# Kernel tuning notes

Measured on AMD Instinct MI355X. Metric: run time of the kernel, lower is better.

## Reference

```python
import jax, jax.numpy as jnp
import numpy as np
import math

B, S, D, H, PD = 2, 2048, 1024, 16, 3
DK = D // H          # 64
SP = S // H          # 128, required so physics_scores matches scores shape


def setup_inputs() -> dict:
    key = jax.random.key(0)
    ks = jax.random.split(key, 16)
    sc = 0.02
    return {
        "query": jax.random.normal(ks[0], (B, S, D), jnp.float32),
        "key_in": jax.random.normal(ks[1], (B, S, D), jnp.float32),
        "value": jax.random.normal(ks[2], (B, S, D), jnp.float32),
        "physics_info": jax.random.normal(ks[3], (B, SP, PD), jnp.float32),
        "Wq": jax.random.normal(ks[4], (D, D), jnp.float32) * sc,
        "bq": jnp.zeros((D,), jnp.float32),
        "Wk": jax.random.normal(ks[5], (D, D), jnp.float32) * sc,
        "bk": jnp.zeros((D,), jnp.float32),
        "Wv": jax.random.normal(ks[6], (D, D), jnp.float32) * sc,
        "bv": jnp.zeros((D,), jnp.float32),
        "Wo": jax.random.normal(ks[7], (D, D), jnp.float32) * sc,
        "bo": jnp.zeros((D,), jnp.float32),
        "Pw": jax.random.normal(ks[8], (PD, D), jnp.float32),   # physics_weight
        "pb": jnp.zeros((1,), jnp.float32),                      # physics_bias
    }


def reference(query, key_in, value, physics_info, Wq, bq, Wk, bk, Wv, bv, Wo, bo, Pw, pb):
    b, s, d = query.shape
    inv = 1.0 / math.sqrt(DK)
    # project and split heads -> [B, H, S, DK]
    Q = (query @ Wq + bq).reshape(b, s, H, DK).transpose(0, 2, 1, 3)
    K = (key_in @ Wk + bk).reshape(b, s, H, DK).transpose(0, 2, 1, 3)
    V = (value @ Wv + bv).reshape(b, s, H, DK).transpose(0, 2, 1, 3)
    scores = jnp.einsum('bhqd,bhkd->bhqk', Q, K) * inv  # [B,H,S,S]
    # physics constraint: [B,SP,D] -> (expand over heads is a no-op) -> [B,SP*H,DK]
    pc = (physics_info @ Pw).reshape(b, SP * H, DK)
    physics_scores = jnp.einsum('bhqd,bkd->bhqk', Q, pc) * inv  # [B,H,S,S]
    scores = scores + pb[0] * physics_scores
    attn = jax.nn.softmax(scores, axis=-1)  # dropout in eval mode (identity)
    ctx = jnp.einsum('bhqk,bhkd->bhqd', attn, V)
    ctx = ctx.transpose(0, 2, 1, 3).reshape(b, s, d)
    return ctx @ Wo + bo
```

## Files before the change

### kernel.cpp

```cpp
#include <hip/hip_runtime.h>
#include <hip/hip_bf16.h>
#include <stdint.h>
#include <math.h>

typedef __bf16 bf16_t;
typedef __attribute__((ext_vector_type(8))) __bf16 bf16x8;
typedef __attribute__((ext_vector_type(4))) __bf16 bf16x4;
typedef __attribute__((ext_vector_type(4))) short short4_t;
typedef __attribute__((ext_vector_type(4))) float f32x4;

#define GLOBAL_AS(p) ((const __attribute__((address_space(1))) void*)(p))
#define LDS_AS(p)    ((__attribute__((address_space(3))) void*)(p))

#define B_ 2
#define S_ 2048
#define D_ 1024
#define H_ 16
#define DK_ 64
#define SP_ 128

#define QSCALE 0.1803368801111144f

static __device__ inline float fast_exp2(float x) {
#if __has_builtin(__builtin_amdgcn_exp2f)
    return __builtin_amdgcn_exp2f(x);
#else
    return __expf(x * 0.6931471805599453f);
#endif
}

static __device__ inline f32x4 mfma16x16x16bf16(short4_t a, short4_t b, f32x4 c) {
#if __has_builtin(__builtin_amdgcn_mfma_f32_16x16x16bf16_1k)
    return __builtin_amdgcn_mfma_f32_16x16x16bf16_1k(a, b, c, 0, 0, 0);
#else
    asm volatile("v_mfma_f32_16x16x16_bf16 %0, %1, %2, %0" : "+v"(c) : "v"(a), "v"(b));
    return c;
#endif
}

struct WPtrs { const float* w[4]; bf16_t* o[4]; };

__global__ __launch_bounds__(256) void prep(
    const float* __restrict__ q, const float* __restrict__ k,
    const float* __restrict__ v,
    bf16_t* __restrict__ qo, bf16_t* __restrict__ ko, bf16_t* __restrict__ vo,
    WPtrs wp, const float* __restrict__ phys, const float* __restrict__ Pw,
    float* __restrict__ PP) {
    int bx = blockIdx.x, tid = threadIdx.x;
    if (bx < 6144) {
        int z = bx >> 11, blk = bx & 2047;
        const float* in = (z == 0) ? q : (z == 1) ? k : v;
        bf16_t* out = (z == 0) ? qo : (z == 1) ? ko : vo;
        size_t i = ((size_t)blk * 256 + tid) * 8;
        f32x4 a = *(const f32x4*)(in + i);
        f32x4 b = *(const f32x4*)(in + i + 4);
        bf16x8 o;
#pragma unroll
        for (int e = 0; e < 4; ++e) { o[e] = (bf16_t)a[e]; o[4 + e] = (bf16_t)b[e]; }
        *(bf16x8*)(out + i) = o;
    } else if (bx < 10240) {
        __shared__ bf16_t t[32][33];
        int idx = bx - 6144;
        int z = idx >> 10;
        const float* W = wp.w[z];
        bf16_t* Wt = wp.o[z];
        int gx = (idx & 31) * 32, gy = ((idx >> 5) & 31) * 32;
        int x = tid & 31, y0 = tid >> 5;
#pragma unroll
        for (int j = 0; j < 32; j += 8)
            t[y0 + j][x] = (bf16_t)W[(size_t)(gy + y0 + j) * D_ + gx + x];
        __syncthreads();
#pragma unroll
        for (int j = 0; j < 32; j += 8)
            Wt[(size_t)(gx + y0 + j) * D_ + gy + x] = t[x][y0 + j];
    } else {
        int i = (bx - 10240) * 256 + tid;
        int n = i & (D_ - 1);
        int sb = i >> 10;
        float acc = 0.f;
#pragma unroll
        for (int p = 0; p < 3; ++p)
            acc += phys[sb * 3 + p] * Pw[p * D_ + n];
        PP[i] = acc;
    }
}

#define GATE(N) do { \
    asm volatile("s_waitcnt vmcnt(" #N ") lgkmcnt(0)" ::: "memory"); \
    __builtin_amdgcn_s_barrier(); \
    __builtin_amdgcn_sched_barrier(0); } while (0)

__global__ __launch_bounds__(512, 2) void qkv_gemm8(
    const bf16_t* __restrict__ Qi, const bf16_t* __restrict__ Ki,
    const bf16_t* __restrict__ Vi,
    const bf16_t* __restrict__ WqT, const bf16_t* __restrict__ WkT,
    const bf16_t* __restrict__ WvT,
    const float* __restrict__ bq, const float* __restrict__ bk,
    const float* __restrict__ bv,
    bf16_t* __restrict__ Qo, bf16_t* __restrict__ Ko, bf16_t* __restrict__ Vo,
    const float* __restrict__ PP, const float* __restrict__ pbp) {
    __shared__ alignas(16) char lds[131072];
    int z = blockIdx.z;
    const bf16_t* A = (z == 0) ? Qi : (z == 1) ? Ki : Vi;
    const bf16_t* Bt = (z == 0) ? WqT : (z == 1) ? WkT : WvT;
    const float* bias = (z == 0) ? bq : (z == 1) ? bk : bv;

    int tid = threadIdx.x;
    int lane = tid & 63, wid = tid >> 6;
    int quad = lane >> 4, l15 = lane & 15;
    int bm = blockIdx.x * 256;
    int bn = blockIdx.y * 256;
    int wm = (wid >> 2) * 128, wn = (wid & 3) * 64;
    const char* gA = (const char*)(A + (size_t)bm * D_);
    const char* gB = (const char*)(Bt + (size_t)bn * D_);
    f32x4 acc[8][4] = {};

    auto STAGE = [&](int t) {
        char* dstA = lds + (t & 3) * 32768;
        char* dstB = dstA + 16384;
        const char* srcA = gA + t * 64;
        const char* srcB = gB + t * 64;
#pragma unroll
        for (int r = 0; r < 2; ++r) {
            int f = r * 8192 + tid * 16;
            int row = f >> 6, col = f & 63;
            __builtin_amdgcn_global_load_lds(GLOBAL_AS(srcA + (size_t)row * (D_ * 2) + col),
                                             LDS_AS(dstA + f), 16, 0, 0);
            __builtin_amdgcn_global_load_lds(GLOBAL_AS(srcB + (size_t)row * (D_ * 2) + col),
                                             LDS_AS(dstB + f), 16, 0, 0);
        }
    };

    STAGE(0); STAGE(1); STAGE(2);

    for (int t = 0; t < 32; ++t) {
        if (t < 30)       GATE(8);
        else if (t == 30) GATE(4);
        else              GATE(0);

        if (t < 29) STAGE(t + 3);

        const char* Ab = lds + (t & 3) * 32768;
        const char* Bb = Ab + 16384;
        bf16x8 af[8], bfr[4];
#pragma unroll
        for (int i = 0; i < 8; ++i)
            af[i] = *(const bf16x8*)(Ab + (wm + i * 16 + l15) * 64 + quad * 16);
#pragma unroll
        for (int j = 0; j < 4; ++j)
            bfr[j] = *(const bf16x8*)(Bb + (wn + j * 16 + l15) * 64 + quad * 16);
#pragma unroll
        for (int i = 0; i < 8; ++i)
#pragma unroll
            for (int j = 0; j < 4; ++j)
                acc[i][j] = __builtin_amdgcn_mfma_f32_16x16x32_bf16(af[i], bfr[j], acc[i][j], 0, 0, 0);
    }

    float pb0 = (z == 1) ? pbp[0] : 0.f;
#pragma unroll
    for (int i = 0; i < 8; ++i)
#pragma unroll
        for (int j = 0; j < 4; ++j) {
            int r0 = bm + wm + i * 16 + quad * 4;
            int c = bn + wn + j * 16 + l15;
            float bv_ = bias[c];
#pragma unroll
            for (int reg = 0; reg < 4; ++reg) {
                int r = r0 + reg;
                float v = acc[i][j][reg] + bv_;
                if (z == 0) {
                    Qo[(size_t)r * D_ + c] = (bf16_t)(v * QSCALE);
                } else if (z == 1) {
                    int b = r >> 11, s = r & (S_ - 1);
                    v += pb0 * PP[((size_t)(b * SP_ + (s >> 4)) << 10) + ((s & 15) << 6) + (c & 63)];
                    Ko[(size_t)r * D_ + c] = (bf16_t)v;
                } else {
                    int b = r >> 11, s = r & (S_ - 1);
                    Vo[(((size_t)b << 10) + c) * S_ + s] = (bf16_t)v;
                }
            }
        }
}

#define KSTR 144
#define VSTR 272

__global__ __launch_bounds__(256) void flash_attn(const bf16_t* Qb,
                                                  const bf16_t* __restrict__ Kb,
                                                  const bf16_t* __restrict__ Vt,
                                                  bf16_t* Ctx) {
    __shared__ alignas(16) char lK[128 * KSTR];
    __shared__ alignas(16) char lV[64 * VSTR];
    int tid = threadIdx.x, lane = tid & 63, wid = tid >> 6;
    int quad = lane >> 4, l15 = lane & 15;
    int q0 = blockIdx.x * 128;
    int h = blockIdx.y, b = blockIdx.z;
    const bf16_t* Qh = Qb + ((size_t)b * S_) * D_ + h * DK_;
    const bf16_t* Kh = Kb + ((size_t)b * S_) * D_ + h * DK_;
    const bf16_t* Vh = Vt + ((size_t)b * D_ + h * DK_) * S_;

    {
        const char* g = (const char*)(Qh + (size_t)q0 * D_);
#pragma unroll
        for (int j = 0; j < 4; ++j) {
            int flat = j * 4096 + tid * 16;
            bf16x8 v = *(const bf16x8*)(g + (size_t)(flat >> 7) * (D_ * 2) + (flat & 127));
            *(bf16x8*)(lK + (flat >> 7) * KSTR + (flat & 127)) = v;
        }
    }
    __syncthreads();
    bf16x8 qf[2][2];
#pragma unroll
    for (int mt = 0; mt < 2; ++mt)
#pragma unroll
        for (int ks = 0; ks < 2; ++ks)
            qf[mt][ks] = *(const bf16x8*)(lK + (wid * 32 + mt * 16 + l15) * KSTR + ks * 64 + quad * 16);

    f32x4 ot[4][2] = {};
    float l_i[2] = {0.f, 0.f};

    for (int t = 0; t < S_ / 128; ++t) {
        const char* gK = (const char*)(Kh + (size_t)t * 128 * D_);
        const char* gV = (const char*)(Vh + (size_t)t * 128);
        bf16x8 vk[4], vv[4];
#pragma unroll
        for (int j = 0; j < 4; ++j) {
            int flat = j * 4096 + tid * 16;
            vk[j] = *(const bf16x8*)(gK + (size_t)(flat >> 7) * (D_ * 2) + (flat & 127));
            vv[j] = *(const bf16x8*)(gV + (size_t)(flat >> 8) * (S_ * 2) + (flat & 255));
        }
        __syncthreads();
#pragma unroll
        for (int j = 0; j < 4; ++j) {
            int flat = j * 4096 + tid * 16;
            *(bf16x8*)(lK + (flat >> 7) * KSTR + (flat & 127)) = vk[j];
            *(bf16x8*)(lV + (flat >> 8) * VSTR + (flat & 255)) = vv[j];
        }
        __syncthreads();

        f32x4 sc[8][2];
#pragma unroll
        for (int kt = 0; kt < 8; ++kt)
#pragma unroll
            for (int mt = 0; mt < 2; ++mt) sc[kt][mt] = (f32x4){0.f, 0.f, 0.f, 0.f};
#pragma unroll
        for (int kt = 0; kt < 8; ++kt) {
            bf16x8 kf0 = *(const bf16x8*)(lK + (kt * 16 + l15) * KSTR + quad * 16);
            bf16x8 kf1 = *(const bf16x8*)(lK + (kt * 16 + l15) * KSTR + 64 + quad * 16);
#pragma unroll
            for (int mt = 0; mt < 2; ++mt) {
                sc[kt][mt] = __builtin_amdgcn_mfma_f32_16x16x32_bf16(kf0, qf[mt][0], sc[kt][mt], 0, 0, 0);
                sc[kt][mt] = __builtin_amdgcn_mfma_f32_16x16x32_bf16(kf1, qf[mt][1], sc[kt][mt], 0, 0, 0);
            }
        }

#pragma unroll
        for (int mt = 0; mt < 2; ++mt) {
            float rsum = 0.f;
#pragma unroll
            for (int kt = 0; kt < 8; ++kt)
#pragma unroll
                for (int r = 0; r < 4; ++r) {
                    float p = fast_exp2(sc[kt][mt][r]);
                    sc[kt][mt][r] = p;
                    rsum += p;
                }
            rsum += __shfl_xor(rsum, 16, 64);
            rsum += __shfl_xor(rsum, 32, 64);
            l_i[mt] += rsum;
        }

#pragma unroll
        for (int kt = 0; kt < 8; ++kt) {
            short4_t bp[2];
#pragma unroll
            for (int mt = 0; mt < 2; ++mt) {
                bf16x4 t4;
#pragma unroll
                for (int r = 0; r < 4; ++r) t4[r] = (bf16_t)sc[kt][mt][r];
                bp[mt] = *(short4_t*)&t4;
            }
#pragma unroll
            for (int dt = 0; dt < 4; ++dt) {
                bf16x4 a4 = *(const bf16x4*)(lV + (dt * 16 + l15) * VSTR + kt * 32 + quad * 8);
                short4_t ap = *(short4_t*)&a4;
#pragma unroll
                for (int mt = 0; mt < 2; ++mt)
                    ot[dt][mt] = mfma16x16x16bf16(ap, bp[mt], ot[dt][mt]);
            }
        }
    }

    __syncthreads();
#pragma unroll
    for (int mt = 0; mt < 2; ++mt) {
        float inv_l = 1.0f / l_i[mt];
#pragma unroll
        for (int dt = 0; dt < 4; ++dt) {
            bf16x4 t4;
#pragma unroll
            for (int r = 0; r < 4; ++r) t4[r] = (bf16_t)(ot[dt][mt][r] * inv_l);
            *(bf16x4*)(lK + (wid * 32 + mt * 16 + l15) * KSTR + dt * 32 + quad * 8) = t4;
        }
    }
    __syncthreads();
    {
        char* gout = (char*)(Ctx + ((size_t)b * S_ + q0) * D_ + h * DK_);
#pragma unroll
        for (int j = 0; j < 4; ++j) {
            int flat = j * 4096 + tid * 16;
            bf16x8 v = *(const bf16x8*)(lK + (flat >> 7) * KSTR + (flat & 127));
            *(bf16x8*)(gout + (size_t)(flat >> 7) * (D_ * 2) + (flat & 127)) = v;
        }
    }
}

__global__ __launch_bounds__(256) void gemm_out(const bf16_t* __restrict__ A,
                                                const bf16_t* __restrict__ Bt,
                                                const float* __restrict__ bias,
                                                float* __restrict__ C) {
    __shared__ alignas(16) bf16_t lA[128 * 64];
    __shared__ alignas(16) bf16_t lB[128 * 64];
    int tid = threadIdx.x;
    int lane = tid & 63, wid = tid >> 6;
    int quad = lane >> 4, l15 = lane & 15;
    int bm = blockIdx.x * 128;
    int bn = blockIdx.y * 128;
    int wm = (wid >> 1) * 64, wn = (wid & 1) * 64;
    f32x4 acc[4][4] = {};

    for (int k0 = 0; k0 < D_; k0 += 64) {
        __syncthreads();
        const char* gA = (const char*)(A + (size_t)bm * D_ + k0);
        const char* gB = (const char*)(Bt + (size_t)bn * D_ + k0);
#pragma unroll
        for (int j = 0; j < 4; ++j) {
            int woff = j * 4096 + wid * 1024;
            int fl = woff + lane * 16;
            int row = fl >> 7, col = fl & 127;
            __builtin_amdgcn_global_load_lds(GLOBAL_AS(gA + (size_t)row * (D_ * 2) + col),
                                             LDS_AS((char*)lA + woff), 16, 0, 0);
            __builtin_amdgcn_global_load_lds(GLOBAL_AS(gB + (size_t)row * (D_ * 2) + col),
                                             LDS_AS((char*)lB + woff), 16, 0, 0);
        }
        __syncthreads();
#pragma unroll
        for (int ks = 0; ks < 2; ++ks) {
            bf16x8 af[4], bfr[4];
#pragma unroll
            for (int i = 0; i < 4; ++i) {
                af[i] = *(const bf16x8*)((const char*)lA + (wm + i * 16 + l15) * 128 + ks * 64 + quad * 16);
                bfr[i] = *(const bf16x8*)((const char*)lB + (wn + i * 16 + l15) * 128 + ks * 64 + quad * 16);
            }
#pragma unroll
            for (int i = 0; i < 4; ++i)
#pragma unroll
                for (int j = 0; j < 4; ++j)
                    acc[i][j] = __builtin_amdgcn_mfma_f32_16x16x32_bf16(af[i], bfr[j], acc[i][j], 0, 0, 0);
        }
    }
#pragma unroll
    for (int i = 0; i < 4; ++i)
#pragma unroll
        for (int j = 0; j < 4; ++j) {
            int r0 = bm + wm + i * 16 + quad * 4;
            int c = bn + wn + j * 16 + l15;
            float bv_ = bias[c];
#pragma unroll
            for (int reg = 0; reg < 4; ++reg)
                C[(size_t)(r0 + reg) * D_ + c] = acc[i][j][reg] + bv_;
        }
}

extern "C" void kernel_launch(void* const* d_in, const int* in_sizes, int n_in,
                              void* d_out, int out_size, void* d_ws, size_t ws_size,
                              hipStream_t stream) {
    const float* query  = (const float*)d_in[0];
    const float* key_in = (const float*)d_in[1];
    const float* value  = (const float*)d_in[2];
    const float* phys   = (const float*)d_in[3];
    const float* Wq     = (const float*)d_in[4];
    const float* bq     = (const float*)d_in[5];
    const float* Wk     = (const float*)d_in[6];
    const float* bk     = (const float*)d_in[7];
    const float* Wv     = (const float*)d_in[8];
    const float* bv     = (const float*)d_in[9];
    const float* Wo     = (const float*)d_in[10];
    const float* bo     = (const float*)d_in[11];
    const float* Pw     = (const float*)d_in[12];
    const float* pb     = (const float*)d_in[13];

    char* ws = (char*)d_ws;
    const size_t MB = 1ull << 20;
    bf16_t* Kb  = (bf16_t*)(ws + 0 * MB);
    bf16_t* QC  = (bf16_t*)(ws + 8 * MB);
    bf16_t* Kin = (bf16_t*)(ws + 16 * MB);
    bf16_t* Vin = (bf16_t*)(ws + 24 * MB);
    bf16_t* WqT = (bf16_t*)(ws + 32 * MB);
    bf16_t* WkT = (bf16_t*)(ws + 34 * MB);
    bf16_t* WvT = (bf16_t*)(ws + 36 * MB);
    bf16_t* WoT = (bf16_t*)(ws + 38 * MB);
    float*  PP  = (float*)(ws + 40 * MB);
    bf16_t* Vt  = (bf16_t*)d_out;
    bf16_t* Qin = (bf16_t*)((char*)d_out + 8 * MB);

    WPtrs wp;
    wp.w[0] = Wq; wp.w[1] = Wk; wp.w[2] = Wv; wp.w[3] = Wo;
    wp.o[0] = WqT; wp.o[1] = WkT; wp.o[2] = WvT; wp.o[3] = WoT;

    prep<<<11264, 256, 0, stream>>>(query, key_in, value, Qin, Kin, Vin,
                                    wp, phys, Pw, PP);

    dim3 gq(16, 4, 3);
    qkv_gemm8<<<gq, 512, 0, stream>>>(Qin, Kin, Vin, WqT, WkT, WvT,
                                      bq, bk, bv, QC, Kb, Vt, PP, pb);

    dim3 fg(S_ / 128, H_, B_);
    flash_attn<<<fg, 256, 0, stream>>>(QC, Kb, Vt, QC);

    dim3 gg(32, 8);
    gemm_out<<<gg, 256, 0, stream>>>(QC, WoT, bo, (float*)d_out);
}
```

Measured before the change: 261.8 us.

## Restructure QKV GEMM to double-buffered K=64 tiles with XOR swizzle and phased MFMA

Replaces the 4-stage, K=32 global_load_lds pipeline with a 2-stage, K=64 pipeline. The new LDS layout uses an XOR swizzle to avoid bank conflicts, and each wave loads only its own half of A and B. The inner loop is split into four phases that interleave fragment loads with MFMA bursts, separated by barriers and s_setprio. V-output stores are vectorised into bf16x4 writes. The intent is to halve loop iterations, reduce LDS bank conflicts and improve store coalescing. The cost is less prefetch depth (vmcnt(0) every iteration) and more barriers.

```diff
diff --git a/kernel.cpp b/kernel.cpp
--- a/kernel.cpp
+++ b/kernel.cpp
@@ -85,11 +85,6 @@
     }
 }
 
-#define GATE(N) do { \
-    asm volatile("s_waitcnt vmcnt(" #N ") lgkmcnt(0)" ::: "memory"); \
-    __builtin_amdgcn_s_barrier(); \
-    __builtin_amdgcn_sched_barrier(0); } while (0)
-
 __global__ __launch_bounds__(512, 2) void qkv_gemm8(
     const bf16_t* __restrict__ Qi, const bf16_t* __restrict__ Ki,
     const bf16_t* __restrict__ Vi,
@@ -115,45 +110,102 @@
     const char* gB = (const char*)(Bt + (size_t)bn * D_);
     f32x4 acc[8][4] = {};
 
+    int hA = wid >> 2;
+    int tgA = tid - hA * 256;
+    int hB = (wid >> 1) & 1;
+    int gB_ = (wid & 1) | ((wid >> 2) << 1);
+    int tgB = gB_ * 64 + lane;
+
     auto STAGE = [&](int t) {
-        char* dstA = lds + (t & 3) * 32768;
-        char* dstB = dstA + 16384;
-        const char* srcA = gA + t * 64;
-        const char* srcB = gB + t * 64;
-#pragma unroll
-        for (int r = 0; r < 2; ++r) {
-            int f = r * 8192 + tid * 16;
-            int row = f >> 6, col = f & 63;
-            __builtin_amdgcn_global_load_lds(GLOBAL_AS(srcA + (size_t)row * (D_ * 2) + col),
-                                             LDS_AS(dstA + f), 16, 0, 0);
-            __builtin_amdgcn_global_load_lds(GLOBAL_AS(srcB + (size_t)row * (D_ * 2) + col),
-                                             LDS_AS(dstB + f), 16, 0, 0);
+        char* bufA = lds + (t & 1) * 65536;
+        char* bufB = bufA + 32768;
+#pragma unroll
+        for (int l = 0; l < 4; ++l) {
+            int L = l * 4096 + tgA * 16;
+            int row = L >> 7, slot = (L >> 4) & 7;
+            int k16 = slot ^ (row & 7);
+            __builtin_amdgcn_global_load_lds(
+                GLOBAL_AS(gA + (size_t)(hA * 128 + row) * (D_ * 2) + t * 128 + k16 * 16),
+                LDS_AS(bufA + hA * 16384 + L), 16, 0, 0);
+        }
+#pragma unroll
+        for (int l = 0; l < 4; ++l) {
+            int L = l * 4096 + tgB * 16;
+            int row = L >> 7, slot = (L >> 4) & 7;
+            int k16 = slot ^ (row & 7);
+            __builtin_amdgcn_global_load_lds(
+                GLOBAL_AS(gB + (size_t)(hB * 128 + row) * (D_ * 2) + t * 128 + k16 * 16),
+                LDS_AS(bufB + hB * 16384 + L), 16, 0, 0);
         }
     };
 
-    STAGE(0); STAGE(1); STAGE(2);
-
-    for (int t = 0; t < 32; ++t) {
-        if (t < 30)       GATE(8);
-        else if (t == 30) GATE(4);
-        else              GATE(0);
-
-        if (t < 29) STAGE(t + 3);
-
-        const char* Ab = lds + (t & 3) * 32768;
-        const char* Bb = Ab + 16384;
-        bf16x8 af[8], bfr[4];
-#pragma unroll
-        for (int i = 0; i < 8; ++i)
-            af[i] = *(const bf16x8*)(Ab + (wm + i * 16 + l15) * 64 + quad * 16);
+    STAGE(0);
+
+    for (int t = 0; t < 16; ++t) {
+        asm volatile("s_waitcnt vmcnt(0)" ::: "memory");
+        __builtin_amdgcn_s_barrier();
+        __builtin_amdgcn_sched_barrier(0);
+
+        if (t < 15) STAGE(t + 1);
+
+        const char* Ab = lds + (t & 1) * 65536 + hA * 16384;
+        const char* Bb = lds + (t & 1) * 65536 + 32768 + hB * 16384;
+
+        bf16x8 bfr[4][2];
+        bf16x8 af[2][2];
+
 #pragma unroll
         for (int j = 0; j < 4; ++j)
-            bfr[j] = *(const bf16x8*)(Bb + (wn + j * 16 + l15) * 64 + quad * 16);
-#pragma unroll
-        for (int i = 0; i < 8; ++i)
+#pragma unroll
+            for (int ks = 0; ks < 2; ++ks) {
+                int row = (wn & 127) + j * 16 + l15;
+                int slot = (ks * 4 + quad) ^ (row & 7);
+                bfr[j][ks] = *(const bf16x8*)(Bb + row * 128 + slot * 16);
+            }
+#pragma unroll
+        for (int ii = 0; ii < 2; ++ii)
+#pragma unroll
+            for (int ks = 0; ks < 2; ++ks) {
+                int row = ii * 16 + l15;
+                int slot = (ks * 4 + quad) ^ (row & 7);
+                af[ii][ks] = *(const bf16x8*)(Ab + row * 128 + slot * 16);
+            }
+        __builtin_amdgcn_s_barrier();
+        __builtin_amdgcn_s_setprio(1);
+#pragma unroll
+        for (int ii = 0; ii < 2; ++ii)
 #pragma unroll
             for (int j = 0; j < 4; ++j)
-                acc[i][j] = __builtin_amdgcn_mfma_f32_16x16x32_bf16(af[i], bfr[j], acc[i][j], 0, 0, 0);
+#pragma unroll
+                for (int ks = 0; ks < 2; ++ks)
+                    acc[ii][j] = __builtin_amdgcn_mfma_f32_16x16x32_bf16(af[ii][ks], bfr[j][ks], acc[ii][j], 0, 0, 0);
+        __builtin_amdgcn_s_setprio(0);
+        __builtin_amdgcn_s_barrier();
+        __builtin_amdgcn_sched_barrier(0);
+
+#pragma unroll
+        for (int p = 1; p < 4; ++p) {
+#pragma unroll
+            for (int ii = 0; ii < 2; ++ii)
+#pragma unroll
+                for (int ks = 0; ks < 2; ++ks) {
+                    int row = (p * 2 + ii) * 16 + l15;
+                    int slot = (ks * 4 + quad) ^ (row & 7);
+                    af[ii][ks] = *(const bf16x8*)(Ab + row * 128 + slot * 16);
+                }
+            __builtin_amdgcn_s_barrier();
+            __builtin_amdgcn_s_setprio(1);
+#pragma unroll
+            for (int ii = 0; ii < 2; ++ii)
+#pragma unroll
+                for (int j = 0; j < 4; ++j)
+#pragma unroll
+                    for (int ks = 0; ks < 2; ++ks)
+                        acc[p * 2 + ii][j] = __builtin_amdgcn_mfma_f32_16x16x32_bf16(af[ii][ks], bfr[j][ks], acc[p * 2 + ii][j], 0, 0, 0);
+            __builtin_amdgcn_s_setprio(0);
+            __builtin_amdgcn_s_barrier();
+            __builtin_amdgcn_sched_barrier(0);
+        }
     }
 
     float pb0 = (z == 1) ? pbp[0] : 0.f;
@@ -164,19 +216,24 @@
             int r0 = bm + wm + i * 16 + quad * 4;
             int c = bn + wn + j * 16 + l15;
             float bv_ = bias[c];
-#pragma unroll
-            for (int reg = 0; reg < 4; ++reg) {
-                int r = r0 + reg;
-                float v = acc[i][j][reg] + bv_;
-                if (z == 0) {
-                    Qo[(size_t)r * D_ + c] = (bf16_t)(v * QSCALE);
-                } else if (z == 1) {
-                    int b = r >> 11, s = r & (S_ - 1);
-                    v += pb0 * PP[((size_t)(b * SP_ + (s >> 4)) << 10) + ((s & 15) << 6) + (c & 63)];
-                    Ko[(size_t)r * D_ + c] = (bf16_t)v;
-                } else {
-                    int b = r >> 11, s = r & (S_ - 1);
-                    Vo[(((size_t)b << 10) + c) * S_ + s] = (bf16_t)v;
+            if (z == 2) {
+                int b = r0 >> 11, s0 = r0 & (S_ - 1);
+                bf16x4 t4;
+#pragma unroll
+                for (int reg = 0; reg < 4; ++reg) t4[reg] = (bf16_t)(acc[i][j][reg] + bv_);
+                *(bf16x4*)(Vo + (((size_t)b << 10) + c) * S_ + s0) = t4;
+            } else {
+#pragma unroll
+                for (int reg = 0; reg < 4; ++reg) {
+                    int r = r0 + reg;
+                    float v = acc[i][j][reg] + bv_;
+                    if (z == 0) {
+                        Qo[(size_t)r * D_ + c] = (bf16_t)(v * QSCALE);
+                    } else {
+                        int b = r >> 11, s = r & (S_ - 1);
+                        v += pb0 * PP[((size_t)(b * SP_ + (s >> 4)) << 10) + ((s & 15) << 6) + (c & 63)];
+                        Ko[(size_t)r * D_ + c] = (bf16_t)v;
+                    }
                 }
             }
         }
```

After: 263.0 us. Within noise of the previous version (+0.4%).
